# Kernel tuning notes

Measured on AMD Instinct MI355X. Metric: run time of the kernel, lower is better.

Reference implementation:

```python
import jax, jax.numpy as jnp
import numpy as np

B, C, H, W = 8, 96, 256, 256
KH, KW = 7, 7


def setup_inputs() -> dict:
    key = jax.random.key(0)
    k1, k2, k3 = jax.random.split(key, 3)
    x = jax.random.normal(k1, (B, C, H, W), dtype=jnp.float32)
    # kaiming_normal fan_out, relu: std = sqrt(2 / fan_out); fan_out = C*k for these shapes
    std_h = float(np.sqrt(2.0 / (C * KH)))
    std_w = float(np.sqrt(2.0 / (C * KW)))
    weight_h = jax.random.normal(k2, (C, 1, KH, 1), dtype=jnp.float32) * std_h
    weight_w = jax.random.normal(k3, (C, 1, 1, KW), dtype=jnp.float32) * std_w
    r = jnp.asarray(1.5, dtype=jnp.float32)  # fractional radius exercises bilinear path
    return {"x": x, "weight_h": weight_h, "weight_w": weight_w, "r": r}


def _axial(x, taps, r, axis):
    """Continuous-offset depthwise conv along one axis.

    x: [B,C,H,W]; taps: [k, C] per-tap depthwise weights; axis: 2 (h) or 3 (w).
    Equivalent to looped grid_sample(align_corners=True, padding_mode='zeros')
    with normalized shift offset*r*2/(size-1), i.e. a pixel shift of offset*r.
    """
    size = x.shape[axis]
    k = taps.shape[0]
    pad = k // 2
    coords = jnp.arange(size, dtype=x.dtype)
    out = jnp.zeros_like(x)
    shp = [1, 1, 1, 1]
    shp[axis] = size
    for i, off in enumerate(range(-pad, pad + 1)):
        pos = coords + off * r                     # sampling position in pixels
        i0f = jnp.floor(pos)
        frac = (pos - i0f).reshape(shp)
        i0 = i0f.astype(jnp.int32)
        i1 = i0 + 1
        m0 = ((i0 >= 0) & (i0 < size)).astype(x.dtype).reshape(shp)
        m1 = ((i1 >= 0) & (i1 < size)).astype(x.dtype).reshape(shp)
        g0 = jnp.take(x, jnp.clip(i0, 0, size - 1), axis=axis) * m0
        g1 = jnp.take(x, jnp.clip(i1, 0, size - 1), axis=axis) * m1
        samp = g0 * (1.0 - frac) + g1 * frac       # bilinear along shifted axis
        out = out + samp * taps[i][None, :, None, None]
    return out


def reference(x, weight_h, weight_w, r):
    # clamp(r, min=1.0) with torch grad semantics (grad 1 at r == 1.0)
    r_val = jnp.where(r < 1.0, jnp.asarray(1.0, x.dtype), r)
    taps_h = weight_h[:, 0, :, 0].T  # [KH, C]
    taps_w = weight_w[:, 0, 0, :].T  # [KW, C]
    return x + _axial(x, taps_h, r_val, 2) + _axial(x, taps_w, r_val, 3)
```

## Files before the change

### kernel.cpp

```cpp
#include <hip/hip_runtime.h>


constexpr int B = 8, C = 96, H = 256, W = 256;
constexpr int KT = 7;
constexpr int HALO = 8;
constexpr int NW = 2 * HALO + 1;
constexpr int RPB = 16;
constexpr int SR = RPB + 2 * HALO;
constexpr int LDW = W + 16;


__global__ __launch_bounds__(64) void build_stencils(
    const float* __restrict__ wh,
    const float* __restrict__ ww,
    const float* __restrict__ rp,
    float* __restrict__ ws)
{
    const int c = blockIdx.x;
    const int d = threadIdx.x;
    if (d >= NW) return;

    float r = rp[0];
    if (r < 1.0f) r = 1.0f;

    float av = 0.f, aw = 0.f;
#pragma unroll
    for (int i = 0; i < KT; ++i) {
        float s   = (float)(i - 3) * r;
        float d0f = floorf(s);
        int   d0  = (int)d0f;
        float f   = s - d0f;
        float thv = wh[c * KT + i];
        float twv = ww[c * KT + i];
        if (d - HALO == d0)     { av = fmaf(thv, 1.f - f, av); aw = fmaf(twv, 1.f - f, aw); }
        if (d - HALO == d0 + 1) { av = fmaf(thv, f, av);       aw = fmaf(twv, f, aw); }
    }
    ws[c * NW + d]          = av;
    ws[C * NW + c * NW + d] = aw;
}

__global__ __launch_bounds__(256, 4) void axialdw_kernel(
    const float* __restrict__ x,
    const float* __restrict__ ws,
    float* __restrict__ out)
{
    __shared__ float tile[SR][LDW];

    constexpr int NWG = B * C * (H / RPB);
    constexpr int CPX = NWG / 8;
    const int bid = blockIdx.x;
    const int lb  = (bid & 7) * CPX + (bid >> 3);

    const int hb   = lb % (H / RPB);
    const int bc   = lb / (H / RPB);
    const int c    = bc % C;
    const int tid  = threadIdx.x;
    const int wave = tid >> 6;
    const int lane = tid & 63;
    const int w0   = lane * 4;

    const float* plane = x + (size_t)bc * (H * W);
    const int gr0 = hb * RPB - HALO;

#pragma unroll
    for (int it = 0; it < SR / 4; ++it) {
        const int i  = wave + 4 * it;
        const int gr = gr0 + i;
        if (gr >= 0 && gr < H) {
            const float* gsrc = plane + (size_t)gr * W + w0;
            __builtin_amdgcn_global_load_lds(
                (const __attribute__((address_space(1))) void*)gsrc,
                (__attribute__((address_space(3))) void*)&tile[i][HALO],
                16, 0, 0);
        } else {
            *(float4*)&tile[i][HALO + w0] = make_float4(0.f, 0.f, 0.f, 0.f);
        }
    }

    if (tid < SR * 4) {
        const int i = tid >> 2;
        const int q = tid & 3;
        const int col = (q < 2) ? q * 4 : (W + (q - 2) * 4 + 8);
        *(float4*)&tile[i][col] = make_float4(0.f, 0.f, 0.f, 0.f);
    }

    float wtv[NW], wth[NW];
#pragma unroll
    for (int d = 0; d < NW; ++d) {
        wtv[d] = ws[c * NW + d];
        wth[d] = ws[C * NW + c * NW + d];
    }

    __syncthreads();

    const int rbase = wave * 4;

    float acc[4][4];
    float ctr[4][4];
#pragma unroll
    for (int rr = 0; rr < 4; ++rr) {
        const float* lrow = &tile[rbase + 8 + rr][w0];
        float sp[20];
#pragma unroll
        for (int k = 0; k < 5; ++k) {
            const float4 v = *(const float4*)(lrow + 4 * k);
            sp[4 * k + 0] = v.x; sp[4 * k + 1] = v.y;
            sp[4 * k + 2] = v.z; sp[4 * k + 3] = v.w;
        }
#pragma unroll
        for (int e = 0; e < 4; ++e) {
            ctr[rr][e] = sp[HALO + e];
            acc[rr][e] = sp[HALO + e];
        }
#pragma unroll
        for (int d = 0; d < NW; ++d) {
            const float wg = wth[d];
            if (wg != 0.f) {
#pragma unroll
                for (int e = 0; e < 4; ++e)
                    acc[rr][e] = fmaf(wg, sp[d + e], acc[rr][e]);
            }
        }
    }

#pragma unroll
    for (int s = 0; s < 20; ++s) {
        float v[4];
        if (s >= 8 && s <= 11) {
#pragma unroll
            for (int e = 0; e < 4; ++e) v[e] = ctr[s - 8][e];
        } else {
            bool need = false;
#pragma unroll
            for (int rr = 0; rr < 4; ++rr) {
                const int d = s - rr;
                if (d >= 0 && d < NW) need = need || (wtv[d] != 0.f);
            }
            if (!need) continue;
            const float4 t = *(const float4*)&tile[rbase + s][HALO + w0];
            v[0] = t.x; v[1] = t.y; v[2] = t.z; v[3] = t.w;
        }
#pragma unroll
        for (int rr = 0; rr < 4; ++rr) {
            const int d = s - rr;
            if (d >= 0 && d < NW) {
                const float wg = wtv[d];
#pragma unroll
                for (int e = 0; e < 4; ++e)
                    acc[rr][e] = fmaf(wg, v[e], acc[rr][e]);
            }
        }
    }

    float* obase = out + (size_t)bc * (H * W)
                 + (size_t)(hb * RPB + rbase) * W + w0;
#pragma unroll
    for (int rr = 0; rr < 4; ++rr) {
        float4 o;
        o.x = acc[rr][0]; o.y = acc[rr][1]; o.z = acc[rr][2]; o.w = acc[rr][3];
        *(float4*)(obase + (size_t)rr * W) = o;
    }
}

extern "C" void kernel_launch(void* const* d_in, const int* in_sizes, int n_in,
                              void* d_out, int out_size, void* d_ws, size_t ws_size,
                              hipStream_t stream) {
    const float* x  = (const float*)d_in[0];
    const float* wh = (const float*)d_in[1];
    const float* ww = (const float*)d_in[2];
    const float* rp = (const float*)d_in[3];
    float* out = (float*)d_out;
    float* ws  = (float*)d_ws;

    build_stencils<<<C, 64, 0, stream>>>(wh, ww, rp, ws);
    const int blocks = B * C * (H / RPB);
    axialdw_kernel<<<blocks, 256, 0, stream>>>(x, ws, out);
}
```

Before: 339.5 us.

## Persistent double-buffered tiles with prefetch and stencil-based halo row skipping

Replaces the one-tile-per-block launch with a persistent grid of 512 blocks, each walking a contiguous run of tiles. The next tile is staged into a second LDS buffer with async global-to-LDS loads while the current one is computed. The stencil builder also records the first and last non-zero vertical offsets per channel, so halo rows that never contribute are not loaded. This aims to hide load latency and cut global traffic, at the cost of doubling LDS per block and reducing occupancy to 2 blocks per SIMD.

Result: slower. 372.3 us (+9.7%).

```diff
diff --git a/kernel.cpp b/kernel.cpp
--- a/kernel.cpp
+++ b/kernel.cpp
@@ -8,6 +8,10 @@
 constexpr int RPB = 16;
 constexpr int SR = RPB + 2 * HALO;
 constexpr int LDW = W + 16;
+constexpr int TILES = B * C * (H / RPB);
+constexpr int GRID = 512;
+constexpr int TPW = TILES / GRID;
+constexpr int TPX = TILES / 8;
 
 
 __global__ __launch_bounds__(64) void build_stencils(
@@ -37,128 +41,151 @@
     }
     ws[c * NW + d]          = av;
     ws[C * NW + c * NW + d] = aw;
+
+    unsigned long long m = __ballot(av != 0.f);
+    if (d == 0) {
+        int lo = 8, hi = 8;
+        if (m) { lo = __ffsll((long long)m) - 1; hi = 63 - __clzll((long long)m); }
+        int* wsi = (int*)ws;
+        wsi[2 * C * NW + 2 * c]     = min(lo, 8);
+        wsi[2 * C * NW + 2 * c + 1] = max(15 + hi, 23);
+    }
 }
 
-__global__ __launch_bounds__(256, 4) void axialdw_kernel(
+__global__ __launch_bounds__(256, 2) void axialdw_kernel(
     const float* __restrict__ x,
     const float* __restrict__ ws,
     float* __restrict__ out)
 {
-    __shared__ float tile[SR][LDW];
-
-    constexpr int NWG = B * C * (H / RPB);
-    constexpr int CPX = NWG / 8;
-    const int bid = blockIdx.x;
-    const int lb  = (bid & 7) * CPX + (bid >> 3);
-
-    const int hb   = lb % (H / RPB);
-    const int bc   = lb / (H / RPB);
-    const int c    = bc % C;
-    const int tid  = threadIdx.x;
-    const int wave = tid >> 6;
-    const int lane = tid & 63;
-    const int w0   = lane * 4;
-
-    const float* plane = x + (size_t)bc * (H * W);
-    const int gr0 = hb * RPB - HALO;
-
-#pragma unroll
-    for (int it = 0; it < SR / 4; ++it) {
-        const int i  = wave + 4 * it;
-        const int gr = gr0 + i;
-        if (gr >= 0 && gr < H) {
-            const float* gsrc = plane + (size_t)gr * W + w0;
-            __builtin_amdgcn_global_load_lds(
-                (const __attribute__((address_space(1))) void*)gsrc,
-                (__attribute__((address_space(3))) void*)&tile[i][HALO],
-                16, 0, 0);
-        } else {
-            *(float4*)&tile[i][HALO + w0] = make_float4(0.f, 0.f, 0.f, 0.f);
-        }
-    }
-
-    if (tid < SR * 4) {
-        const int i = tid >> 2;
-        const int q = tid & 3;
-        const int col = (q < 2) ? q * 4 : (W + (q - 2) * 4 + 8);
-        *(float4*)&tile[i][col] = make_float4(0.f, 0.f, 0.f, 0.f);
-    }
-
-    float wtv[NW], wth[NW];
-#pragma unroll
-    for (int d = 0; d < NW; ++d) {
-        wtv[d] = ws[c * NW + d];
-        wth[d] = ws[C * NW + c * NW + d];
-    }
-
-    __syncthreads();
-
+    __shared__ __align__(16) float tile[2][SR][LDW];
+
+    const int g     = blockIdx.x;
+    const int tbase = (g & 7) * TPX + (g >> 3) * TPW;
+    const int tid   = threadIdx.x;
+    const int wave  = tid >> 6;
+    const int lane  = tid & 63;
+    const int w0    = lane * 4;
     const int rbase = wave * 4;
-
-    float acc[4][4];
-    float ctr[4][4];
-#pragma unroll
-    for (int rr = 0; rr < 4; ++rr) {
-        const float* lrow = &tile[rbase + 8 + rr][w0];
-        float sp[20];
-#pragma unroll
-        for (int k = 0; k < 5; ++k) {
-            const float4 v = *(const float4*)(lrow + 4 * k);
-            sp[4 * k + 0] = v.x; sp[4 * k + 1] = v.y;
-            sp[4 * k + 2] = v.z; sp[4 * k + 3] = v.w;
-        }
-#pragma unroll
-        for (int e = 0; e < 4; ++e) {
-            ctr[rr][e] = sp[HALO + e];
-            acc[rr][e] = sp[HALO + e];
-        }
+    const int* wsi  = (const int*)ws;
+
+    {
+        const int q    = tid & 3;
+        const int i    = (tid >> 2) & 31;
+        const int bsel = tid >> 7;
+        const int col  = (q < 2) ? q * 4 : (W + 8 + (q - 2) * 4);
+        *(float4*)&tile[bsel][i][col] = make_float4(0.f, 0.f, 0.f, 0.f);
+    }
+
+    auto stage = [&](float (*buf)[LDW], int t) {
+        const int hb = t & 15;
+        const int bc = t >> 4;
+        const int c  = bc % C;
+        const int smin = wsi[2 * C * NW + 2 * c];
+        const int smax = wsi[2 * C * NW + 2 * c + 1];
+        const float* plane = x + (size_t)bc * (H * W);
+        const int gr0 = hb * RPB - HALO;
+#pragma unroll
+        for (int it = 0; it < SR / 4; ++it) {
+            const int i = wave + 4 * it;
+            if (i < smin || i > smax) continue;
+            const int gr = gr0 + i;
+            if (gr >= 0 && gr < H) {
+                const float* gsrc = plane + (size_t)gr * W + w0;
+                __builtin_amdgcn_global_load_lds(
+                    (const __attribute__((address_space(1))) void*)gsrc,
+                    (__attribute__((address_space(3))) void*)&buf[i][HALO],
+                    16, 0, 0);
+            } else {
+                *(float4*)&buf[i][HALO + w0] = make_float4(0.f, 0.f, 0.f, 0.f);
+            }
+        }
+    };
+
+    auto compute_store = [&](const float (*buf)[LDW], int t) {
+        const int hb = t & 15;
+        const int bc = t >> 4;
+        const int c  = bc % C;
+
+        float wtv[NW], wth[NW];
 #pragma unroll
         for (int d = 0; d < NW; ++d) {
-            const float wg = wth[d];
-            if (wg != 0.f) {
-#pragma unroll
-                for (int e = 0; e < 4; ++e)
-                    acc[rr][e] = fmaf(wg, sp[d + e], acc[rr][e]);
-            }
-        }
-    }
-
-#pragma unroll
-    for (int s = 0; s < 20; ++s) {
-        float v[4];
-        if (s >= 8 && s <= 11) {
-#pragma unroll
-            for (int e = 0; e < 4; ++e) v[e] = ctr[s - 8][e];
-        } else {
-            bool need = false;
+            wtv[d] = ws[c * NW + d];
+            wth[d] = ws[C * NW + c * NW + d];
+        }
+
+        float acc[4][4], ctr[4][4];
+#pragma unroll
+        for (int rr = 0; rr < 4; ++rr) {
+            const float* lrow = &buf[rbase + 8 + rr][w0];
+            float sp[20];
+#pragma unroll
+            for (int k = 0; k < 5; ++k) {
+                const float4 v = *(const float4*)(lrow + 4 * k);
+                sp[4 * k + 0] = v.x; sp[4 * k + 1] = v.y;
+                sp[4 * k + 2] = v.z; sp[4 * k + 3] = v.w;
+            }
+#pragma unroll
+            for (int e = 0; e < 4; ++e) {
+                ctr[rr][e] = sp[HALO + e];
+                acc[rr][e] = sp[HALO + e];
+            }
+#pragma unroll
+            for (int d = 0; d < NW; ++d) {
+                const float wg = wth[d];
+                if (wg != 0.f) {
+#pragma unroll
+                    for (int e = 0; e < 4; ++e)
+                        acc[rr][e] = fmaf(wg, sp[d + e], acc[rr][e]);
+                }
+            }
+        }
+
+#pragma unroll
+        for (int s = 0; s < 20; ++s) {
+            float v[4];
+            if (s >= 8 && s <= 11) {
+#pragma unroll
+                for (int e = 0; e < 4; ++e) v[e] = ctr[s - 8][e];
+            } else {
+                bool need = false;
+#pragma unroll
+                for (int rr = 0; rr < 4; ++rr) {
+                    const int d = s - rr;
+                    if (d >= 0 && d < NW) need = need || (wtv[d] != 0.f);
+                }
+                if (!need) continue;
+                const float4 tv = *(const float4*)&buf[rbase + s][HALO + w0];
+                v[0] = tv.x; v[1] = tv.y; v[2] = tv.z; v[3] = tv.w;
+            }
 #pragma unroll
             for (int rr = 0; rr < 4; ++rr) {
                 const int d = s - rr;
-                if (d >= 0 && d < NW) need = need || (wtv[d] != 0.f);
-            }
-            if (!need) continue;
-            const float4 t = *(const float4*)&tile[rbase + s][HALO + w0];
-            v[0] = t.x; v[1] = t.y; v[2] = t.z; v[3] = t.w;
-        }
+                if (d >= 0 && d < NW) {
+                    const float wg = wtv[d];
+#pragma unroll
+                    for (int e = 0; e < 4; ++e)
+                        acc[rr][e] = fmaf(wg, v[e], acc[rr][e]);
+                }
+            }
+        }
+
+        float* obase = out + (size_t)bc * (H * W)
+                     + (size_t)(hb * RPB + rbase) * W + w0;
 #pragma unroll
         for (int rr = 0; rr < 4; ++rr) {
-            const int d = s - rr;
-            if (d >= 0 && d < NW) {
-                const float wg = wtv[d];
-#pragma unroll
-                for (int e = 0; e < 4; ++e)
-                    acc[rr][e] = fmaf(wg, v[e], acc[rr][e]);
-            }
-        }
-    }
-
-    float* obase = out + (size_t)bc * (H * W)
-                 + (size_t)(hb * RPB + rbase) * W + w0;
-#pragma unroll
-    for (int rr = 0; rr < 4; ++rr) {
-        float4 o;
-        o.x = acc[rr][0]; o.y = acc[rr][1]; o.z = acc[rr][2]; o.w = acc[rr][3];
-        *(float4*)(obase + (size_t)rr * W) = o;
+            float4 o;
+            o.x = acc[rr][0]; o.y = acc[rr][1]; o.z = acc[rr][2]; o.w = acc[rr][3];
+            *(float4*)(obase + (size_t)rr * W) = o;
+        }
+    };
+
+    stage(tile[0], tbase);
+    __syncthreads();
+#pragma unroll 2
+    for (int k = 0; k < TPW; ++k) {
+        if (k + 1 < TPW) stage(tile[(k + 1) & 1], tbase + k + 1);
+        compute_store(tile[k & 1], tbase + k);
+        __syncthreads();
     }
 }
 
@@ -173,6 +200,5 @@
     float* ws  = (float*)d_ws;
 
     build_stencils<<<C, 64, 0, stream>>>(wh, ww, rp, ws);
-    const int blocks = B * C * (H / RPB);
-    axialdw_kernel<<<blocks, 256, 0, stream>>>(x, ws, out);
+    axialdw_kernel<<<GRID, 256, 0, stream>>>(x, ws, out);
 }
```

## Use 32-row tiles with 512 threads and skip halo rows unused by stencil

Applied to the files above, without the earlier changes.

Doubles the rows per block to 32 and the threads to 512, which lowers the fraction of halo rows loaded per output row. The stencil builder now records the span of nonzero vertical taps per channel so the load loop skips halo rows that no tap reads. The vertical pass is reordered to run before the horizontal pass, which removes the saved centre values. With larger blocks and more LDS per block, occupancy may change, and the skipped rows hold uninitialized LDS that is never read.

Measured after the change: 342.0 us. No clear change (+0.7%).

```diff
diff --git a/kernel.cpp b/kernel.cpp
--- a/kernel.cpp
+++ b/kernel.cpp
@@ -5,9 +5,11 @@
 constexpr int KT = 7;
 constexpr int HALO = 8;
 constexpr int NW = 2 * HALO + 1;
-constexpr int RPB = 16;
+constexpr int RPB = 32;
 constexpr int SR = RPB + 2 * HALO;
 constexpr int LDW = W + 16;
+constexpr int TILES = B * C * (H / RPB);
+constexpr int TPX = TILES / 8;
 
 
 __global__ __launch_bounds__(64) void build_stencils(
@@ -37,34 +39,56 @@
     }
     ws[c * NW + d]          = av;
     ws[C * NW + c * NW + d] = aw;
+
+    unsigned long long m = __ballot(av != 0.f);
+    if (d == 0) {
+        int lo = HALO, hi = HALO;
+        if (m) { lo = __ffsll((long long)m) - 1; hi = 63 - __clzll((long long)m); }
+        int* wsi = (int*)ws;
+        wsi[2 * C * NW + 2 * c]     = lo;
+        wsi[2 * C * NW + 2 * c + 1] = hi;
+    }
 }
 
-__global__ __launch_bounds__(256, 4) void axialdw_kernel(
+__global__ __launch_bounds__(512, 6) void axialdw_kernel(
     const float* __restrict__ x,
     const float* __restrict__ ws,
     float* __restrict__ out)
 {
-    __shared__ float tile[SR][LDW];
+    __shared__ __align__(16) float tile[SR][LDW];
 
-    constexpr int NWG = B * C * (H / RPB);
-    constexpr int CPX = NWG / 8;
     const int bid = blockIdx.x;
-    const int lb  = (bid & 7) * CPX + (bid >> 3);
+    const int lb  = (bid & 7) * TPX + (bid >> 3);
 
-    const int hb   = lb % (H / RPB);
-    const int bc   = lb / (H / RPB);
+    const int hb   = lb & (H / RPB - 1);
+    const int bc   = lb >> 3;
     const int c    = bc % C;
     const int tid  = threadIdx.x;
     const int wave = tid >> 6;
     const int lane = tid & 63;
     const int w0   = lane * 4;
+    const int rbase = wave * 4;
+
+    const int* wsi  = (const int*)ws;
+    const int lo    = wsi[2 * C * NW + 2 * c];
+    const int hi    = wsi[2 * C * NW + 2 * c + 1];
+    const int smin  = min(lo, HALO);
+    const int smax  = max(RPB - 1 + hi, RPB + 7);
 
     const float* plane = x + (size_t)bc * (H * W);
     const int gr0 = hb * RPB - HALO;
 
+    if (tid < SR * 4) {
+        const int i   = tid >> 2;
+        const int q   = tid & 3;
+        const int col = (q < 2) ? q * 4 : (W + 8 + (q - 2) * 4);
+        *(float4*)&tile[i][col] = make_float4(0.f, 0.f, 0.f, 0.f);
+    }
+
 #pragma unroll
-    for (int it = 0; it < SR / 4; ++it) {
-        const int i  = wave + 4 * it;
+    for (int it = 0; it < SR / 8; ++it) {
+        const int i = wave + 8 * it;
+        if (i < smin || i > smax) continue;
         const int gr = gr0 + i;
         if (gr >= 0 && gr < H) {
             const float* gsrc = plane + (size_t)gr * W + w0;
@@ -77,13 +101,6 @@
         }
     }
 
-    if (tid < SR * 4) {
-        const int i = tid >> 2;
-        const int q = tid & 3;
-        const int col = (q < 2) ? q * 4 : (W + (q - 2) * 4 + 8);
-        *(float4*)&tile[i][col] = make_float4(0.f, 0.f, 0.f, 0.f);
-    }
-
     float wtv[NW], wth[NW];
 #pragma unroll
     for (int d = 0; d < NW; ++d) {
@@ -93,10 +110,38 @@
 
     __syncthreads();
 
-    const int rbase = wave * 4;
+    float acc[4][4];
+#pragma unroll
+    for (int rr = 0; rr < 4; ++rr)
+#pragma unroll
+        for (int e = 0; e < 4; ++e) acc[rr][e] = 0.f;
 
-    float acc[4][4];
-    float ctr[4][4];
+#pragma unroll
+    for (int t = 0; t < 20; ++t) {
+        bool need = false;
+#pragma unroll
+        for (int rr = 0; rr < 4; ++rr) {
+            const int d = t - rr;
+            if (d >= 0 && d < NW) need = need || (wtv[d] != 0.f);
+        }
+        if (!need) continue;
+        const float4 v = *(const float4*)&tile[rbase + t][HALO + w0];
+#pragma unroll
+        for (int rr = 0; rr < 4; ++rr) {
+            const int d = t - rr;
+            if (d >= 0 && d < NW) {
+                const float wg = wtv[d];
+#pragma unroll
+                for (int e = 0; e < 4; ++e) {
+                    const float s = (&v.x)[e];
+                    acc[rr][e] = fmaf(wg, s, acc[rr][e]);
+                }
+            }
+        }
+    }
+
+    float* obase = out + (size_t)bc * (H * W)
+                 + (size_t)(hb * RPB + rbase) * W + w0;
 #pragma unroll
     for (int rr = 0; rr < 4; ++rr) {
         const float* lrow = &tile[rbase + 8 + rr][w0];
@@ -108,10 +153,8 @@
             sp[4 * k + 2] = v.z; sp[4 * k + 3] = v.w;
         }
 #pragma unroll
-        for (int e = 0; e < 4; ++e) {
-            ctr[rr][e] = sp[HALO + e];
-            acc[rr][e] = sp[HALO + e];
-        }
+        for (int e = 0; e < 4; ++e)
+            acc[rr][e] += sp[HALO + e];
 #pragma unroll
         for (int d = 0; d < NW; ++d) {
             const float wg = wth[d];
@@ -121,41 +164,6 @@
                     acc[rr][e] = fmaf(wg, sp[d + e], acc[rr][e]);
             }
         }
-    }
-
-#pragma unroll
-    for (int s = 0; s < 20; ++s) {
-        float v[4];
-        if (s >= 8 && s <= 11) {
-#pragma unroll
-            for (int e = 0; e < 4; ++e) v[e] = ctr[s - 8][e];
-        } else {
-            bool need = false;
-#pragma unroll
-            for (int rr = 0; rr < 4; ++rr) {
-                const int d = s - rr;
-                if (d >= 0 && d < NW) need = need || (wtv[d] != 0.f);
-            }
-            if (!need) continue;
-            const float4 t = *(const float4*)&tile[rbase + s][HALO + w0];
-            v[0] = t.x; v[1] = t.y; v[2] = t.z; v[3] = t.w;
-        }
-#pragma unroll
-        for (int rr = 0; rr < 4; ++rr) {
-            const int d = s - rr;
-            if (d >= 0 && d < NW) {
-                const float wg = wtv[d];
-#pragma unroll
-                for (int e = 0; e < 4; ++e)
-                    acc[rr][e] = fmaf(wg, v[e], acc[rr][e]);
-            }
-        }
-    }
-
-    float* obase = out + (size_t)bc * (H * W)
-                 + (size_t)(hb * RPB + rbase) * W + w0;
-#pragma unroll
-    for (int rr = 0; rr < 4; ++rr) {
         float4 o;
         o.x = acc[rr][0]; o.y = acc[rr][1]; o.z = acc[rr][2]; o.w = acc[rr][3];
         *(float4*)(obase + (size_t)rr * W) = o;
@@ -173,6 +181,5 @@
     float* ws  = (float*)d_ws;
 
     build_stencils<<<C, 64, 0, stream>>>(wh, ww, rp, ws);
-    const int blocks = B * C * (H / RPB);
-    axialdw_kernel<<<blocks, 256, 0, stream>>>(x, ws, out);
+    axialdw_kernel<<<TILES, 512, 0, stream>>>(x, ws, out);
 }
```
